# Kernel tuning notes

Measured on AMD Instinct MI355X. Metric: run time of the kernel, lower is better.

The kernel has to match this reference:

```python
import jax, jax.numpy as jnp
import numpy as np

NUM_ITERATIONS = 5
EPSILON_0 = 1.0
EPS = 1e-20


def setup_inputs() -> dict:
    key = jax.random.key(0)
    k1, k2 = jax.random.split(key)
    B, NIN, NOUT = 8192, 3072, 512
    x = jax.random.uniform(k1, (B, NIN), dtype=jnp.float32)
    w = jax.random.uniform(k2, (NOUT, NIN), dtype=jnp.float32)
    # weights setter normalizes rows to sum to 1
    w = w / w.sum(axis=1, keepdims=True)
    h_initial = jnp.full((NOUT,), 1.0 / NOUT, dtype=jnp.float32)
    return {"x": x, "weights": w, "h_initial": h_initial}


def reference(x, weights, h_initial):
    # x: [B, NIN], weights: [NOUT, NIN], h_initial: [NOUT]
    x = x / (x.sum(axis=1, keepdims=True) + EPS)  # input normalization in forward()
    B = x.shape[0]
    h = jnp.broadcast_to(h_initial[None, :], (B, h_initial.shape[0]))

    def step(h, _):
        # Original: h_w = h[:,:,None]*W[None]; h_w /= h_w.sum(1,keepdim)+eps;
        #           h_w = (h_w * x[:,None,:]).sum(-1)
        # Equivalent without materializing [B, NOUT, NIN]:
        denom = h @ weights                       # [B, NIN] = sum_n h_bn W_nk
        h_w = h * ((x / (denom + EPS)) @ weights.T)  # [B, NOUT]
        h_new = h + EPSILON_0 * h_w               # epsilon_0 > 0 branch
        h_new = h_new / (h_new.sum(axis=1, keepdims=True) + EPS)
        return h_new, None

    h, _ = jax.lax.scan(step, h, None, length=NUM_ITERATIONS)
    return h
```

## Files before the change

### kernel.cpp

```cpp
#include <hip/hip_runtime.h>


#define NIN 3072
#define NOUT 512

using f32x4  = __attribute__((ext_vector_type(4))) float;

__device__ __forceinline__ unsigned short f2bf(float f) {
    unsigned int u = __builtin_bit_cast(unsigned int, f);
    return (unsigned short)((u + 0x7fffu + ((u >> 16) & 1u)) >> 16);
}
__device__ __forceinline__ float bf2f(unsigned short s) {
    unsigned int u = ((unsigned int)s) << 16;
    return __builtin_bit_cast(float, u);
}

#define LDS_BARRIER() do {                                   \
    asm volatile("s_waitcnt lgkmcnt(0)" ::: "memory");       \
    __builtin_amdgcn_s_barrier();                            \
    asm volatile("" ::: "memory");                           \
} while (0)

__global__ void prep_all(const float* __restrict__ x,
                         const float* __restrict__ W,
                         const float* __restrict__ h_init,
                         unsigned short* __restrict__ X2,
                         unsigned char* __restrict__ W1,
                         unsigned char* __restrict__ W2,
                         float* __restrict__ d0inv) {
    __shared__ float wsum[4];
    __shared__ float dred[8][32];
    const int bb = blockIdx.x;
    const int t  = threadIdx.x;

    if (bb < 8192) {
        const int b = bb;
        const float4* r4 = reinterpret_cast<const float4*>(x + (size_t)b * NIN);
        float s = 0.f;
        float4 v0 = r4[t], v1 = r4[t + 256], v2 = r4[t + 512];
        s = v0.x + v0.y + v0.z + v0.w + v1.x + v1.y + v1.z + v1.w + v2.x + v2.y + v2.z + v2.w;
        #pragma unroll
        for (int off = 32; off > 0; off >>= 1) s += __shfl_down(s, off, 64);
        int w = t >> 6, l = t & 63;
        if (l == 0) wsum[w] = s;
        __syncthreads();
        float inv = 1.0f / (wsum[0] + wsum[1] + wsum[2] + wsum[3] + 1e-20f);
        unsigned short* orow = X2 + (size_t)b * NIN;
        #pragma unroll
        for (int c = 0; c < 3; ++c) {
            float4 v = (c == 0) ? v0 : (c == 1) ? v1 : v2;
            ushort4 o;
            o.x = f2bf(v.x * inv); o.y = f2bf(v.y * inv);
            o.z = f2bf(v.z * inv); o.w = f2bf(v.w * inv);
            *reinterpret_cast<ushort4*>(orow + (t + c * 256) * 4) = o;
        }
    } else if (bb < 8192 + 1152) {
        int tt = (bb - 8192) * 256 + t;
        if (tt < 98304) {
            int f = tt >> 6, l = tt & 63;
            int kcg = f >> 4, pr = f & 15;
            int kbase = kcg * 32 + ((l >> 4) << 3);
            unsigned int words[4];
            #pragma unroll
            for (int h8 = 0; h8 < 2; ++h8) {
                int n = (pr * 2 + h8) * 16 + (l & 15);
                const float* src = W + (size_t)n * NIN + kbase;
                float v[8];
                #pragma unroll
                for (int j = 0; j < 8; ++j) v[j] = src[j] * 4096.0f;
                int lo32 = __builtin_amdgcn_cvt_pk_fp8_f32(v[0], v[1], 0, false);
                lo32     = __builtin_amdgcn_cvt_pk_fp8_f32(v[2], v[3], lo32, true);
                int hi32 = __builtin_amdgcn_cvt_pk_fp8_f32(v[4], v[5], 0, false);
                hi32     = __builtin_amdgcn_cvt_pk_fp8_f32(v[6], v[7], hi32, true);
                words[h8 * 2]     = (unsigned int)lo32;
                words[h8 * 2 + 1] = (unsigned int)hi32;
            }
            *reinterpret_cast<uint4*>(W2 + (size_t)tt * 16) =
                *reinterpret_cast<uint4*>(words);
        } else {
            int u = tt - 98304;
            int f = u >> 6, l = u & 63;
            int ktg = f >> 4, nc = f & 15;
            int k = ktg * 16 + (l & 15);
            int nb = nc * 32 + ((l >> 4) << 3);
            float v[8];
            #pragma unroll
            for (int j = 0; j < 8; ++j) v[j] = W[(size_t)(nb + j) * NIN + k] * 4096.0f;
            int lo32 = __builtin_amdgcn_cvt_pk_fp8_f32(v[0], v[1], 0, false);
            lo32     = __builtin_amdgcn_cvt_pk_fp8_f32(v[2], v[3], lo32, true);
            int hi32 = __builtin_amdgcn_cvt_pk_fp8_f32(v[4], v[5], 0, false);
            hi32     = __builtin_amdgcn_cvt_pk_fp8_f32(v[6], v[7], hi32, true);
            uint2 o; o.x = (unsigned int)lo32; o.y = (unsigned int)hi32;
            *reinterpret_cast<uint2*>(W1 + (size_t)u * 8) = o;
        }
    } else {
        int kb = bb - 9344;
        int kid = t & 31, nsub = t >> 5;
        int k = kb * 32 + kid;
        int n0 = nsub * 64;
        float s = 0.f;
        const float* p = W + (size_t)n0 * NIN + k;
        #pragma unroll 8
        for (int n = 0; n < 64; ++n) s += h_init[n0 + n] * p[(size_t)n * NIN];
        dred[nsub][kid] = s;
        __syncthreads();
        if (t < 32) {
            float sm = 1e-20f;
            #pragma unroll
            for (int j = 0; j < 8; ++j) sm += dred[j][t];
            d0inv[kb * 32 + t] = 1.0f / sm;
        }
    }
}

__global__ __launch_bounds__(512)
__attribute__((amdgpu_waves_per_eu(2, 2)))
void nnmf_main(
    const unsigned short* __restrict__ X2,
    const unsigned char* __restrict__ W1,
    const unsigned char* __restrict__ W2,
    const float* __restrict__ d0inv,
    const float* __restrict__ h_init,
    float* __restrict__ out)
{
    __shared__ unsigned char  h8_lds[32 * 528];
    __shared__ unsigned short x_lds[32 * 136];
    __shared__ unsigned char  r8_lds[32 * 144];
    __shared__ float red[8][32];

    const int tid = threadIdx.x;
    const int w  = tid >> 6;
    const int l  = tid & 63;
    const int lo = l & 15;
    const int hi = l >> 4;
    const int b0 = blockIdx.x * 32;

    float h_reg[2][4][4];
    #pragma unroll
    for (int nt = 0; nt < 4; ++nt) {
        float hv = h_init[w * 64 + nt * 16 + lo];
        #pragma unroll
        for (int m = 0; m < 2; ++m)
            #pragma unroll
            for (int i = 0; i < 4; ++i)
                h_reg[m][nt][i] = hv;
    }

    const int xrow = tid >> 4, xcc = tid & 15;
    const uint4* xg = reinterpret_cast<const uint4*>(X2 + (size_t)(b0 + xrow) * NIN + xcc * 8);
    unsigned short* xdst = &x_lds[xrow * 136 + xcc * 8];

    const unsigned char* w1base = W1 + ((size_t)(w * 16)) * 512 + (size_t)l * 8;
    const unsigned char* w2base = W2 + (size_t)(w * 2) * 1024 + (size_t)l * 16;

    *reinterpret_cast<uint4*>(xdst) = xg[0];
    uint4 xnext = xg[16];
    long long w1buf[16];
    long long hfr[2][16];
    __syncthreads();

    const float DSCL = 9.5367431640625e-07f;
    const float TS   = 1.0f / 65536.0f;
    f32x4 tacc[2][4];

    for (int it = 0; it < 5; ++it) {
        if (it != 0) {
            #pragma unroll
            for (int m = 0; m < 2; ++m)
                #pragma unroll
                for (int nc = 0; nc < 16; ++nc)
                    hfr[m][nc] = *reinterpret_cast<const long long*>(
                        &h8_lds[(m * 16 + lo) * 528 + nc * 32 + hi * 8]);
        }

        #pragma unroll
        for (int m = 0; m < 2; ++m)
            #pragma unroll
            for (int nt = 0; nt < 4; ++nt)
                tacc[m][nt] = (f32x4){0.f, 0.f, 0.f, 0.f};

        for (int s = 0; s < 24; ++s) {
            const int sn  = (s + 1 == 24) ? 0 : s + 1;
            const int sn2 = (s + 2 >= 24) ? (s + 2 - 24) : s + 2;

            uint4 xfut = xg[sn2 * 16];

            uint4 w2v[8];
            {
                const unsigned char* w2p = w2base + (size_t)s * 65536;
                #pragma unroll
                for (int kc = 0; kc < 4; ++kc)
                    #pragma unroll
                    for (int p = 0; p < 2; ++p)
                        w2v[kc * 2 + p] = *reinterpret_cast<const uint4*>(
                            w2p + (size_t)kc * 16384 + p * 1024);
            }

            f32x4 d0, d1;
            float dv = 0.f;
            if (it == 0) {
                dv = d0inv[s * 128 + w * 16 + lo];
            } else {
                f32x4 a0a = {0,0,0,0}, a0b = {0,0,0,0}, a1a = {0,0,0,0}, a1b = {0,0,0,0};
                #pragma unroll
                for (int nc = 0; nc < 16; nc += 2) {
                    a0a = __builtin_amdgcn_mfma_f32_16x16x32_fp8_fp8(hfr[0][nc],     w1buf[nc],     a0a, 0, 0, 0);
                    a1a = __builtin_amdgcn_mfma_f32_16x16x32_fp8_fp8(hfr[1][nc],     w1buf[nc],     a1a, 0, 0, 0);
                    a0b = __builtin_amdgcn_mfma_f32_16x16x32_fp8_fp8(hfr[0][nc + 1], w1buf[nc + 1], a0b, 0, 0, 0);
                    a1b = __builtin_amdgcn_mfma_f32_16x16x32_fp8_fp8(hfr[1][nc + 1], w1buf[nc + 1], a1b, 0, 0, 0);
                }
                d0 = a0a + a0b;
                d1 = a1a + a1b;
            }

            #pragma unroll
            for (int i = 0; i < 4; ++i) {
                int row0 = hi * 4 + i;
                float x0 = bf2f(x_lds[row0 * 136 + w * 16 + lo]) * 16.0f;
                float x1 = bf2f(x_lds[(16 + row0) * 136 + w * 16 + lo]) * 16.0f;
                float r0, r1;
                if (it == 0) { r0 = x0 * dv; r1 = x1 * dv; }
                else {
                    r0 = x0 * __builtin_amdgcn_rcpf(fmaf(d0[i], DSCL, 1e-20f));
                    r1 = x1 * __builtin_amdgcn_rcpf(fmaf(d1[i], DSCL, 1e-20f));
                }
                int c0 = __builtin_amdgcn_cvt_pk_fp8_f32(r0, r0, 0, false);
                int c1 = __builtin_amdgcn_cvt_pk_fp8_f32(r1, r1, 0, false);
                r8_lds[row0 * 144 + w * 16 + lo] = (unsigned char)(c0 & 0xff);
                r8_lds[(16 + row0) * 144 + w * 16 + lo] = (unsigned char)(c1 & 0xff);
            }
            LDS_BARRIER();

            #pragma unroll
            for (int kc = 0; kc < 2; ++kc) {
                long long ra0 = *reinterpret_cast<const long long*>(&r8_lds[lo * 144 + kc * 32 + hi * 8]);
                long long ra1 = *reinterpret_cast<const long long*>(&r8_lds[(16 + lo) * 144 + kc * 32 + hi * 8]);
                #pragma unroll
                for (int p = 0; p < 2; ++p) {
                    union { uint4 v; long long q[2]; } u;
                    u.v = w2v[kc * 2 + p];
                    #pragma unroll
                    for (int h8 = 0; h8 < 2; ++h8) {
                        int nt = p * 2 + h8;
                        tacc[0][nt] = __builtin_amdgcn_mfma_f32_16x16x32_fp8_fp8(ra0, u.q[h8], tacc[0][nt], 0, 0, 0);
                        tacc[1][nt] = __builtin_amdgcn_mfma_f32_16x16x32_fp8_fp8(ra1, u.q[h8], tacc[1][nt], 0, 0, 0);
                    }
                }
            }

            if (it > 0 || s == 23) {
                const unsigned char* w1p = w1base + (size_t)sn * 65536;
                #pragma unroll
                for (int nc = 0; nc < 16; ++nc)
                    w1buf[nc] = *reinterpret_cast<const long long*>(w1p + (size_t)nc * 512);
            }

            #pragma unroll
            for (int kc = 2; kc < 4; ++kc) {
                long long ra0 = *reinterpret_cast<const long long*>(&r8_lds[lo * 144 + kc * 32 + hi * 8]);
                long long ra1 = *reinterpret_cast<const long long*>(&r8_lds[(16 + lo) * 144 + kc * 32 + hi * 8]);
                #pragma unroll
                for (int p = 0; p < 2; ++p) {
                    union { uint4 v; long long q[2]; } u;
                    u.v = w2v[kc * 2 + p];
                    #pragma unroll
                    for (int h8 = 0; h8 < 2; ++h8) {
                        int nt = p * 2 + h8;
                        tacc[0][nt] = __builtin_amdgcn_mfma_f32_16x16x32_fp8_fp8(ra0, u.q[h8], tacc[0][nt], 0, 0, 0);
                        tacc[1][nt] = __builtin_amdgcn_mfma_f32_16x16x32_fp8_fp8(ra1, u.q[h8], tacc[1][nt], 0, 0, 0);
                    }
                }
            }

            *reinterpret_cast<uint4*>(xdst) = xnext;
            xnext = xfut;
            LDS_BARRIER();
        }

        float p[2][4];
        #pragma unroll
        for (int m = 0; m < 2; ++m)
            #pragma unroll
            for (int i = 0; i < 4; ++i) p[m][i] = 0.f;

        #pragma unroll
        for (int m = 0; m < 2; ++m)
            #pragma unroll
            for (int nt = 0; nt < 4; ++nt)
                #pragma unroll
                for (int i = 0; i < 4; ++i) {
                    float v = h_reg[m][nt][i] * (1.f + tacc[m][nt][i] * TS);
                    h_reg[m][nt][i] = v;
                    p[m][i] += v;
                }
        #pragma unroll
        for (int mask = 1; mask < 16; mask <<= 1)
            #pragma unroll
            for (int m = 0; m < 2; ++m)
                #pragma unroll
                for (int i = 0; i < 4; ++i)
                    p[m][i] += __shfl_xor(p[m][i], mask, 64);
        if (lo == 0) {
            #pragma unroll
            for (int m = 0; m < 2; ++m)
                #pragma unroll
                for (int i = 0; i < 4; ++i)
                    red[w][m * 16 + hi * 4 + i] = p[m][i];
        }
        __syncthreads();
        float inv[2][4];
        #pragma unroll
        for (int m = 0; m < 2; ++m)
            #pragma unroll
            for (int i = 0; i < 4; ++i) {
                int row = m * 16 + hi * 4 + i;
                float S = 0.f;
                #pragma unroll
                for (int ww = 0; ww < 8; ++ww) S += red[ww][row];
                inv[m][i] = 1.f / (S + 1e-20f);
            }

        if (it < 4) {
            #pragma unroll
            for (int m = 0; m < 2; ++m)
                #pragma unroll
                for (int nt = 0; nt < 4; ++nt)
                    #pragma unroll
                    for (int i = 0; i < 4; ++i) {
                        int row = m * 16 + hi * 4 + i;
                        int col = w * 64 + nt * 16 + lo;
                        float hv = h_reg[m][nt][i] * inv[m][i];
                        h_reg[m][nt][i] = hv;
                        int c = __builtin_amdgcn_cvt_pk_fp8_f32(hv * 256.0f, hv * 256.0f, 0, false);
                        h8_lds[row * 528 + col] = (unsigned char)(c & 0xff);
                    }
            __syncthreads();
        } else {
            #pragma unroll
            for (int m = 0; m < 2; ++m)
                #pragma unroll
                for (int nt = 0; nt < 4; ++nt)
                    #pragma unroll
                    for (int i = 0; i < 4; ++i) {
                        int row = m * 16 + hi * 4 + i;
                        int col = w * 64 + nt * 16 + lo;
                        out[(size_t)(b0 + row) * 512 + col] = h_reg[m][nt][i] * inv[m][i];
                    }
        }
    }
}

extern "C" void kernel_launch(void* const* d_in, const int* in_sizes, int n_in,
                              void* d_out, int out_size, void* d_ws, size_t ws_size,
                              hipStream_t stream) {
    const float* x   = (const float*)d_in[0];
    const float* wgt = (const float*)d_in[1];
    const float* h0  = (const float*)d_in[2];
    float* out = (float*)d_out;

    unsigned short* X2 = (unsigned short*)d_ws;
    unsigned char*  W1 = (unsigned char*)((char*)d_ws + 50331648);
    unsigned char*  W2 = (unsigned char*)((char*)d_ws + 51904512);
    float* d0inv       = (float*)((char*)d_ws + 53477376);

    prep_all<<<9440, 256, 0, stream>>>(x, wgt, h0, X2, W1, W2, d0inv);
    nnmf_main<<<256, 512, 0, stream>>>(X2, W1, W2, d0inv, h0, out);
}
```

Before: 470.0 us.

## Switch fp8 MFMAs to 16x16x128 scaled variant with repacked weight layouts

Replaces the 16x16x32 fp8 MFMA chains in both GEMMs with the MI355X 16x16x128 f8f6f4 scaled MFMA using unit scales. The prep kernel repacks W1 and W2 into 32-byte-per-lane fragments to match, and h fragments are now read from LDS per step instead of held in registers for the whole iteration. This cuts the MFMA instruction count and the register pressure from hfr, at the cost of extra LDS reads each step. It also changes the launch bounds from an explicit waves-per-EU setting to a min-blocks hint.

```diff
diff --git a/kernel.cpp b/kernel.cpp
--- a/kernel.cpp
+++ b/kernel.cpp
@@ -4,7 +4,14 @@
 #define NIN 3072
 #define NOUT 512
 
-using f32x4  = __attribute__((ext_vector_type(4))) float;
+using f32x4 = __attribute__((ext_vector_type(4))) float;
+using i32x8 = __attribute__((ext_vector_type(8))) int;
+
+union frag32 { i32x8 v; uint4 q[2]; };
+
+#define MFMA128(A, B, C) \
+    __builtin_amdgcn_mfma_scale_f32_16x16x128_f8f6f4( \
+        (A), (B), (C), 0, 0, 0, (int)0x7f7f7f7f, 0, (int)0x7f7f7f7f)
 
 __device__ __forceinline__ unsigned short f2bf(float f) {
     unsigned int u = __builtin_bit_cast(unsigned int, f);
@@ -54,47 +61,49 @@
             o.z = f2bf(v.z * inv); o.w = f2bf(v.w * inv);
             *reinterpret_cast<ushort4*>(orow + (t + c * 256) * 4) = o;
         }
-    } else if (bb < 8192 + 1152) {
+    } else if (bb < 8192 + 384) {
         int tt = (bb - 8192) * 256 + t;
-        if (tt < 98304) {
-            int f = tt >> 6, l = tt & 63;
-            int kcg = f >> 4, pr = f & 15;
-            int kbase = kcg * 32 + ((l >> 4) << 3);
-            unsigned int words[4];
-            #pragma unroll
-            for (int h8 = 0; h8 < 2; ++h8) {
-                int n = (pr * 2 + h8) * 16 + (l & 15);
-                const float* src = W + (size_t)n * NIN + kbase;
-                float v[8];
-                #pragma unroll
-                for (int j = 0; j < 8; ++j) v[j] = src[j] * 4096.0f;
-                int lo32 = __builtin_amdgcn_cvt_pk_fp8_f32(v[0], v[1], 0, false);
-                lo32     = __builtin_amdgcn_cvt_pk_fp8_f32(v[2], v[3], lo32, true);
-                int hi32 = __builtin_amdgcn_cvt_pk_fp8_f32(v[4], v[5], 0, false);
-                hi32     = __builtin_amdgcn_cvt_pk_fp8_f32(v[6], v[7], hi32, true);
-                words[h8 * 2]     = (unsigned int)lo32;
-                words[h8 * 2 + 1] = (unsigned int)hi32;
-            }
-            *reinterpret_cast<uint4*>(W2 + (size_t)tt * 16) =
-                *reinterpret_cast<uint4*>(words);
+        unsigned int words[8];
+        if (tt < 49152) {
+            int l = tt & 63, g = tt >> 6;
+            int s = g >> 5, rem = g & 31, w = rem >> 2, nt = rem & 3;
+            int n = w * 64 + nt * 16 + (l & 15);
+            int kbase = s * 128 + ((l >> 4) << 5);
+            const float* src = W + (size_t)n * NIN + kbase;
+            #pragma unroll
+            for (int q = 0; q < 8; ++q) {
+                float v0 = src[q * 4 + 0] * 4096.0f, v1 = src[q * 4 + 1] * 4096.0f;
+                float v2 = src[q * 4 + 2] * 4096.0f, v3 = src[q * 4 + 3] * 4096.0f;
+                int pk = __builtin_amdgcn_cvt_pk_fp8_f32(v0, v1, 0, false);
+                pk     = __builtin_amdgcn_cvt_pk_fp8_f32(v2, v3, pk, true);
+                words[q] = (unsigned int)pk;
+            }
+            uint4* dst = reinterpret_cast<uint4*>(W2 + (size_t)tt * 32);
+            dst[0] = *reinterpret_cast<uint4*>(&words[0]);
+            dst[1] = *reinterpret_cast<uint4*>(&words[4]);
         } else {
-            int u = tt - 98304;
-            int f = u >> 6, l = u & 63;
-            int ktg = f >> 4, nc = f & 15;
-            int k = ktg * 16 + (l & 15);
-            int nb = nc * 32 + ((l >> 4) << 3);
-            float v[8];
-            #pragma unroll
-            for (int j = 0; j < 8; ++j) v[j] = W[(size_t)(nb + j) * NIN + k] * 4096.0f;
-            int lo32 = __builtin_amdgcn_cvt_pk_fp8_f32(v[0], v[1], 0, false);
-            lo32     = __builtin_amdgcn_cvt_pk_fp8_f32(v[2], v[3], lo32, true);
-            int hi32 = __builtin_amdgcn_cvt_pk_fp8_f32(v[4], v[5], 0, false);
-            hi32     = __builtin_amdgcn_cvt_pk_fp8_f32(v[6], v[7], hi32, true);
-            uint2 o; o.x = (unsigned int)lo32; o.y = (unsigned int)hi32;
-            *reinterpret_cast<uint2*>(W1 + (size_t)u * 8) = o;
+            int u = tt - 49152;
+            int l = u & 63, g = u >> 6;
+            int c = g & 3, sw = g >> 2;
+            int w = sw & 7, s = sw >> 3;
+            int kout = s * 128 + w * 16 + (l & 15);
+            int nbase = c * 128 + ((l >> 4) << 5);
+            #pragma unroll
+            for (int q = 0; q < 8; ++q) {
+                float v0 = W[(size_t)(nbase + q * 4 + 0) * NIN + kout] * 4096.0f;
+                float v1 = W[(size_t)(nbase + q * 4 + 1) * NIN + kout] * 4096.0f;
+                float v2 = W[(size_t)(nbase + q * 4 + 2) * NIN + kout] * 4096.0f;
+                float v3 = W[(size_t)(nbase + q * 4 + 3) * NIN + kout] * 4096.0f;
+                int pk = __builtin_amdgcn_cvt_pk_fp8_f32(v0, v1, 0, false);
+                pk     = __builtin_amdgcn_cvt_pk_fp8_f32(v2, v3, pk, true);
+                words[q] = (unsigned int)pk;
+            }
+            uint4* dst = reinterpret_cast<uint4*>(W1 + (size_t)u * 32);
+            dst[0] = *reinterpret_cast<uint4*>(&words[0]);
+            dst[1] = *reinterpret_cast<uint4*>(&words[4]);
         }
     } else {
-        int kb = bb - 9344;
+        int kb = bb - 8576;
         int kid = t & 31, nsub = t >> 5;
         int k = kb * 32 + kid;
         int n0 = nsub * 64;
@@ -113,9 +122,7 @@
     }
 }
 
-__global__ __launch_bounds__(512)
-__attribute__((amdgpu_waves_per_eu(2, 2)))
-void nnmf_main(
+__global__ __launch_bounds__(512, 1) void nnmf_main(
     const unsigned short* __restrict__ X2,
     const unsigned char* __restrict__ W1,
     const unsigned char* __restrict__ W2,
@@ -150,13 +157,12 @@
     const uint4* xg = reinterpret_cast<const uint4*>(X2 + (size_t)(b0 + xrow) * NIN + xcc * 8);
     unsigned short* xdst = &x_lds[xrow * 136 + xcc * 8];
 
-    const unsigned char* w1base = W1 + ((size_t)(w * 16)) * 512 + (size_t)l * 8;
-    const unsigned char* w2base = W2 + (size_t)(w * 2) * 1024 + (size_t)l * 16;
+    const unsigned char* w1base = W1 + (size_t)w * 8192 + (size_t)l * 32;
+    const unsigned char* w2base = W2 + ((size_t)(w * 4) * 64 + l) * 32;
 
     *reinterpret_cast<uint4*>(xdst) = xg[0];
     uint4 xnext = xg[16];
-    long long w1buf[16];
-    long long hfr[2][16];
+    frag32 w1buf[4];
     __syncthreads();
 
     const float DSCL = 9.5367431640625e-07f;
@@ -164,15 +170,6 @@
     f32x4 tacc[2][4];
 
     for (int it = 0; it < 5; ++it) {
-        if (it != 0) {
-            #pragma unroll
-            for (int m = 0; m < 2; ++m)
-                #pragma unroll
-                for (int nc = 0; nc < 16; ++nc)
-                    hfr[m][nc] = *reinterpret_cast<const long long*>(
-                        &h8_lds[(m * 16 + lo) * 528 + nc * 32 + hi * 8]);
-        }
-
         #pragma unroll
         for (int m = 0; m < 2; ++m)
             #pragma unroll
@@ -185,15 +182,15 @@
 
             uint4 xfut = xg[sn2 * 16];
 
-            uint4 w2v[8];
+            frag32 w2v[4];
             {
                 const unsigned char* w2p = w2base + (size_t)s * 65536;
                 #pragma unroll
-                for (int kc = 0; kc < 4; ++kc)
-                    #pragma unroll
-                    for (int p = 0; p < 2; ++p)
-                        w2v[kc * 2 + p] = *reinterpret_cast<const uint4*>(
-                            w2p + (size_t)kc * 16384 + p * 1024);
+                for (int nt = 0; nt < 4; ++nt) {
+                    const uint4* p = reinterpret_cast<const uint4*>(w2p + nt * 2048);
+                    w2v[nt].q[0] = p[0];
+                    w2v[nt].q[1] = p[1];
+                }
             }
 
             f32x4 d0, d1;
@@ -201,16 +198,21 @@
             if (it == 0) {
                 dv = d0inv[s * 128 + w * 16 + lo];
             } else {
-                f32x4 a0a = {0,0,0,0}, a0b = {0,0,0,0}, a1a = {0,0,0,0}, a1b = {0,0,0,0};
-                #pragma unroll
-                for (int nc = 0; nc < 16; nc += 2) {
-                    a0a = __builtin_amdgcn_mfma_f32_16x16x32_fp8_fp8(hfr[0][nc],     w1buf[nc],     a0a, 0, 0, 0);
-                    a1a = __builtin_amdgcn_mfma_f32_16x16x32_fp8_fp8(hfr[1][nc],     w1buf[nc],     a1a, 0, 0, 0);
-                    a0b = __builtin_amdgcn_mfma_f32_16x16x32_fp8_fp8(hfr[0][nc + 1], w1buf[nc + 1], a0b, 0, 0, 0);
-                    a1b = __builtin_amdgcn_mfma_f32_16x16x32_fp8_fp8(hfr[1][nc + 1], w1buf[nc + 1], a1b, 0, 0, 0);
-                }
-                d0 = a0a + a0b;
-                d1 = a1a + a1b;
+                f32x4 a0 = {0,0,0,0}, a1 = {0,0,0,0};
+                #pragma unroll
+                for (int c = 0; c < 4; ++c) {
+                    frag32 ha0, ha1;
+                    const uint4* p0 = reinterpret_cast<const uint4*>(
+                        &h8_lds[lo * 528 + c * 128 + hi * 32]);
+                    const uint4* p1 = reinterpret_cast<const uint4*>(
+                        &h8_lds[(16 + lo) * 528 + c * 128 + hi * 32]);
+                    ha0.q[0] = p0[0]; ha0.q[1] = p0[1];
+                    ha1.q[0] = p1[0]; ha1.q[1] = p1[1];
+                    a0 = MFMA128(ha0.v, w1buf[c].v, a0);
+                    a1 = MFMA128(ha1.v, w1buf[c].v, a1);
+                }
+                d0 = a0;
+                d1 = a1;
             }
 
             #pragma unroll
@@ -231,45 +233,32 @@
             }
             LDS_BARRIER();
 
-            #pragma unroll
-            for (int kc = 0; kc < 2; ++kc) {
-                long long ra0 = *reinterpret_cast<const long long*>(&r8_lds[lo * 144 + kc * 32 + hi * 8]);
-                long long ra1 = *reinterpret_cast<const long long*>(&r8_lds[(16 + lo) * 144 + kc * 32 + hi * 8]);
-                #pragma unroll
-                for (int p = 0; p < 2; ++p) {
-                    union { uint4 v; long long q[2]; } u;
-                    u.v = w2v[kc * 2 + p];
-                    #pragma unroll
-                    for (int h8 = 0; h8 < 2; ++h8) {
-                        int nt = p * 2 + h8;
-                        tacc[0][nt] = __builtin_amdgcn_mfma_f32_16x16x32_fp8_fp8(ra0, u.q[h8], tacc[0][nt], 0, 0, 0);
-                        tacc[1][nt] = __builtin_amdgcn_mfma_f32_16x16x32_fp8_fp8(ra1, u.q[h8], tacc[1][nt], 0, 0, 0);
-                    }
-                }
+            {
+                frag32 ra;
+                const uint4* p = reinterpret_cast<const uint4*>(&r8_lds[lo * 144 + hi * 32]);
+                ra.q[0] = p[0]; ra.q[1] = p[1];
+                #pragma unroll
+                for (int nt = 0; nt < 4; ++nt)
+                    tacc[0][nt] = MFMA128(ra.v, w2v[nt].v, tacc[0][nt]);
             }
 
             if (it > 0 || s == 23) {
                 const unsigned char* w1p = w1base + (size_t)sn * 65536;
                 #pragma unroll
-                for (int nc = 0; nc < 16; ++nc)
-                    w1buf[nc] = *reinterpret_cast<const long long*>(w1p + (size_t)nc * 512);
-            }
-
-            #pragma unroll
-            for (int kc = 2; kc < 4; ++kc) {
-                long long ra0 = *reinterpret_cast<const long long*>(&r8_lds[lo * 144 + kc * 32 + hi * 8]);
-                long long ra1 = *reinterpret_cast<const long long*>(&r8_lds[(16 + lo) * 144 + kc * 32 + hi * 8]);
-                #pragma unroll
-                for (int p = 0; p < 2; ++p) {
-                    union { uint4 v; long long q[2]; } u;
-                    u.v = w2v[kc * 2 + p];
-                    #pragma unroll
-                    for (int h8 = 0; h8 < 2; ++h8) {
-                        int nt = p * 2 + h8;
-                        tacc[0][nt] = __builtin_amdgcn_mfma_f32_16x16x32_fp8_fp8(ra0, u.q[h8], tacc[0][nt], 0, 0, 0);
-                        tacc[1][nt] = __builtin_amdgcn_mfma_f32_16x16x32_fp8_fp8(ra1, u.q[h8], tacc[1][nt], 0, 0, 0);
-                    }
-                }
+                for (int c = 0; c < 4; ++c) {
+                    const uint4* p = reinterpret_cast<const uint4*>(w1p + c * 2048);
+                    w1buf[c].q[0] = p[0];
+                    w1buf[c].q[1] = p[1];
+                }
+            }
+
+            {
+                frag32 ra;
+                const uint4* p = reinterpret_cast<const uint4*>(&r8_lds[(16 + lo) * 144 + hi * 32]);
+                ra.q[0] = p[0]; ra.q[1] = p[1];
+                #pragma unroll
+                for (int nt = 0; nt < 4; ++nt)
+                    tacc[1][nt] = MFMA128(ra.v, w2v[nt].v, tacc[1][nt]);
             }
 
             *reinterpret_cast<uint4*>(xdst) = xnext;
@@ -363,6 +352,6 @@
     unsigned char*  W2 = (unsigned char*)((char*)d_ws + 51904512);
     float* d0inv       = (float*)((char*)d_ws + 53477376);
 
-    prep_all<<<9440, 256, 0, stream>>>(x, wgt, h0, X2, W1, W2, d0inv);
+    prep_all<<<8672, 256, 0, stream>>>(x, wgt, h0, X2, W1, W2, d0inv);
     nnmf_main<<<256, 512, 0, stream>>>(X2, W1, W2, d0inv, h0, out);
 }
```

New measurement: 400.1 us. -14.9%, faster.
